# Optimization experiments

Hardware: AMD Instinct MI355X
Metric: run time of the kernel (lower is better)

Reference implementation:

```python
import jax, jax.numpy as jnp
import numpy as np

H = 64          # hidden_dim
G = 4           # grid_size
NB = 4.0        # neighborhood
PRED = 12       # pred_steps


def _social_pool(all_h, positions, idx, W_sp, b_sp):
    """Vectorized grid-based social pooling. all_h:(N,H), positions:(N,2) -> (H,)."""
    N = positions.shape[0]
    pos_i = positions[idx]
    diff = positions - pos_i                                   # (N,2)
    in_nb = jnp.max(jnp.abs(diff), axis=1) <= NB
    mask = in_nb & (jnp.arange(N) != idx)
    # torch: int(clamp(((d/NB)+1)/2 * G, 0, G-1)); truncation==floor after clip here
    g = jnp.clip(jnp.floor((diff / NB + 1.0) / 2.0 * G), 0, G - 1).astype(jnp.int32)
    cell = g[:, 1] * G + g[:, 0]                               # gy*G + gx, (N,)
    m = mask.astype(all_h.dtype)[:, None]                      # (N,1)
    grid = jax.ops.segment_sum(all_h * m, cell, num_segments=G * G)   # (16,H)
    counts = jax.ops.segment_sum(m, cell, num_segments=G * G)         # (16,1)
    pooled = (grid / jnp.maximum(counts, 1.0)).sum(axis=0)            # (H,)
    return pooled @ W_sp.T + b_sp


def _lstm_cell(inp, h, c, W_ih, b_ih, W_hh, b_hh):
    gates = inp @ W_ih.T + b_ih + h @ W_hh.T + b_hh            # (4H,)
    i, f, g, o = jnp.split(gates, 4)
    i, f, o = jax.nn.sigmoid(i), jax.nn.sigmoid(f), jax.nn.sigmoid(o)
    g = jnp.tanh(g)
    c_new = f * c + i * g
    return o * jnp.tanh(c_new), c_new


def setup_inputs() -> dict:
    key = jax.random.key(0)
    ks = jax.random.split(key, 10)
    N, T = 2_000_000, 8
    s = 0.05
    return {
        "history": jax.random.normal(ks[0], (T, 4), jnp.float32),
        "all_h": jax.random.normal(ks[1], (N, H), jnp.float32),
        "positions": jax.random.normal(ks[2], (N, 2), jnp.float32) * 3.0,
        "W_in": jax.random.normal(ks[3], (H, 4), jnp.float32) * s,
        "b_in": jnp.zeros((H,), jnp.float32),
        "W_ih": jax.random.normal(ks[4], (4 * H, 2 * H), jnp.float32) * s,
        "b_ih": jnp.zeros((4 * H,), jnp.float32),
        "W_hh": jax.random.normal(ks[5], (4 * H, H), jnp.float32) * s,
        "b_hh": jnp.zeros((4 * H,), jnp.float32),
        "W_sp": jax.random.normal(ks[6], (H, H), jnp.float32) * s,
        "b_sp": jnp.zeros((H,), jnp.float32),
        "W_out": jax.random.normal(ks[7], (2, H), jnp.float32) * s,
        "b_out": jnp.zeros((2,), jnp.float32),
        "idx": 0,
    }


def reference(history, all_h, positions, W_in, b_in, W_ih, b_ih, W_hh, b_hh,
              W_sp, b_sp, W_out, b_out, idx):
    # all_h, positions, idx are fixed inputs, so the social vector is identical
    # at every timestep (same math as recomputing it each step in the original).
    social = _social_pool(all_h, positions, idx, W_sp, b_sp)   # (H,)

    def enc_step(carry, x):
        h, c = carry
        emb = x @ W_in.T + b_in
        inp = jnp.concatenate([emb, social])
        h, c = _lstm_cell(inp, h, c, W_ih, b_ih, W_hh, b_hh)
        return (h, c), None

    h0 = jnp.zeros((H,), history.dtype)
    (h, c), _ = jax.lax.scan(enc_step, (h0, h0), history)

    last_pos = history[-1, :2]

    def pred_step(carry, _):
        h, c, lp = carry
        delta = h @ W_out.T + b_out                            # (2,)
        vel = delta / 0.5
        x = jnp.concatenate([lp + delta, vel])                 # (4,)
        emb = x @ W_in.T + b_in
        inp = jnp.concatenate([emb, social])
        h, c = _lstm_cell(inp, h, c, W_ih, b_ih, W_hh, b_hh)
        return (h, c, lp + delta), delta

    _, preds = jax.lax.scan(pred_step, (h, c, last_pos), None, length=PRED)
    return preds  # (pred_steps, 2)
```

## Files before the change

kernel.cpp:

```cpp
#include <hip/hip_runtime.h>

#define HDIM 64
#define CELLS 16
#define WPB 4
#define PV (CELLS * HDIM + CELLS)

#define WS_M1K   1040
#define WS_G0    2064
#define WS_SINK  2320
#define WS_PART  2576

__global__ void __launch_bounds__(256) k_pool(
    const float* __restrict__ all_h, const float2* __restrict__ pos2,
    const int* __restrict__ idxp, float* __restrict__ partial,
    int N, int nwaves)
{
    __shared__ float acc[WPB][CELLS * HDIM];
    __shared__ float cnt[WPB][CELLS];
    __shared__ __align__(16) int lst[WPB][64];
    const int tid  = threadIdx.x;
    const int wave = tid >> 6;
    const int lane = tid & 63;

    for (int v = tid; v < WPB * CELLS * HDIM; v += 256) ((float*)acc)[v] = 0.0f;
    if (tid < WPB * CELLS) ((float*)cnt)[tid] = 0.0f;
    __syncthreads();

    const int    idx0 = idxp[0];
    const float2 p0   = pos2[idx0];
    const int    gw   = blockIdx.x * WPB + wave;
    float* __restrict__ accw = acc[wave];
    int*   __restrict__ lstw = lst[wave];

    for (int base = gw * 64; base < N; base += nwaves * 64) {
        const int a = base + lane;
        int cellid = -1;
        if (a < N && a != idx0) {
            const float2 p = pos2[a];
            const float dx = p.x - p0.x;
            const float dy = p.y - p0.y;
            if (fmaxf(fabsf(dx), fabsf(dy)) <= 4.0f) {
                const float f0 = floorf((dx / 4.0f + 1.0f) / 2.0f * 4.0f);
                const float f1 = floorf((dy / 4.0f + 1.0f) / 2.0f * 4.0f);
                const int g0 = (int)fminf(fmaxf(f0, 0.0f), 3.0f);
                const int g1 = (int)fminf(fmaxf(f1, 0.0f), 3.0f);
                cellid = g1 * 4 + g0;
                atomicAdd(&cnt[wave][cellid], 1.0f);
            }
        }
        const unsigned long long mask  = __ballot(cellid >= 0);
        const int                M     = __popcll(mask);
        const unsigned long long below = mask & ((1ULL << lane) - 1ULL);
        if (cellid >= 0) lstw[__popcll(below)] = (lane << 4) | cellid;

        const float* __restrict__ rowp = all_h + (size_t)base * HDIM + lane;
        int r = 0;
        for (; r + 16 <= M; r += 16) {
            const int4 e0 = *(const int4*)&lstw[r];
            const int4 e1 = *(const int4*)&lstw[r + 4];
            const int4 e2 = *(const int4*)&lstw[r + 8];
            const int4 e3 = *(const int4*)&lstw[r + 12];
            const float v0  = rowp[(size_t)(e0.x >> 4) * HDIM];
            const float v1  = rowp[(size_t)(e0.y >> 4) * HDIM];
            const float v2  = rowp[(size_t)(e0.z >> 4) * HDIM];
            const float v3  = rowp[(size_t)(e0.w >> 4) * HDIM];
            const float v4  = rowp[(size_t)(e1.x >> 4) * HDIM];
            const float v5  = rowp[(size_t)(e1.y >> 4) * HDIM];
            const float v6  = rowp[(size_t)(e1.z >> 4) * HDIM];
            const float v7  = rowp[(size_t)(e1.w >> 4) * HDIM];
            const float v8  = rowp[(size_t)(e2.x >> 4) * HDIM];
            const float v9  = rowp[(size_t)(e2.y >> 4) * HDIM];
            const float v10 = rowp[(size_t)(e2.z >> 4) * HDIM];
            const float v11 = rowp[(size_t)(e2.w >> 4) * HDIM];
            const float v12 = rowp[(size_t)(e3.x >> 4) * HDIM];
            const float v13 = rowp[(size_t)(e3.y >> 4) * HDIM];
            const float v14 = rowp[(size_t)(e3.z >> 4) * HDIM];
            const float v15 = rowp[(size_t)(e3.w >> 4) * HDIM];
            accw[(e0.x & 15) * HDIM + lane] += v0;
            accw[(e0.y & 15) * HDIM + lane] += v1;
            accw[(e0.z & 15) * HDIM + lane] += v2;
            accw[(e0.w & 15) * HDIM + lane] += v3;
            accw[(e1.x & 15) * HDIM + lane] += v4;
            accw[(e1.y & 15) * HDIM + lane] += v5;
            accw[(e1.z & 15) * HDIM + lane] += v6;
            accw[(e1.w & 15) * HDIM + lane] += v7;
            accw[(e2.x & 15) * HDIM + lane] += v8;
            accw[(e2.y & 15) * HDIM + lane] += v9;
            accw[(e2.z & 15) * HDIM + lane] += v10;
            accw[(e2.w & 15) * HDIM + lane] += v11;
            accw[(e3.x & 15) * HDIM + lane] += v12;
            accw[(e3.y & 15) * HDIM + lane] += v13;
            accw[(e3.z & 15) * HDIM + lane] += v14;
            accw[(e3.w & 15) * HDIM + lane] += v15;
        }
        for (; r + 8 <= M; r += 8) {
            const int4 e0 = *(const int4*)&lstw[r];
            const int4 e1 = *(const int4*)&lstw[r + 4];
            const float v0 = rowp[(size_t)(e0.x >> 4) * HDIM];
            const float v1 = rowp[(size_t)(e0.y >> 4) * HDIM];
            const float v2 = rowp[(size_t)(e0.z >> 4) * HDIM];
            const float v3 = rowp[(size_t)(e0.w >> 4) * HDIM];
            const float v4 = rowp[(size_t)(e1.x >> 4) * HDIM];
            const float v5 = rowp[(size_t)(e1.y >> 4) * HDIM];
            const float v6 = rowp[(size_t)(e1.z >> 4) * HDIM];
            const float v7 = rowp[(size_t)(e1.w >> 4) * HDIM];
            accw[(e0.x & 15) * HDIM + lane] += v0;
            accw[(e0.y & 15) * HDIM + lane] += v1;
            accw[(e0.z & 15) * HDIM + lane] += v2;
            accw[(e0.w & 15) * HDIM + lane] += v3;
            accw[(e1.x & 15) * HDIM + lane] += v4;
            accw[(e1.y & 15) * HDIM + lane] += v5;
            accw[(e1.z & 15) * HDIM + lane] += v6;
            accw[(e1.w & 15) * HDIM + lane] += v7;
        }
        for (; r < M; ++r) {
            const int e = lstw[r];
            accw[(e & 15) * HDIM + lane] += rowp[(size_t)(e >> 4) * HDIM];
        }
    }
    __syncthreads();

    float* __restrict__ outp = partial + (size_t)blockIdx.x * PV;
    for (int v = tid; v < CELLS * HDIM; v += 256)
        outp[v] = acc[0][v] + acc[1][v] + acc[2][v] + acc[3][v];
    if (tid < CELLS)
        outp[CELLS * HDIM + tid] = cnt[0][tid] + cnt[1][tid] + cnt[2][tid] + cnt[3][tid];
}

__global__ void __launch_bounds__(256) k_reduce(
    const float* __restrict__ partial, float* __restrict__ ws,
    const float* __restrict__ W_in, const float* __restrict__ b_in,
    const float* __restrict__ W_ih, const float* __restrict__ b_ih,
    const float* __restrict__ W_hh, const float* __restrict__ b_hh,
    const float* __restrict__ W_sp, const float* __restrict__ W_out,
    int nbp)
{
    const int tid = threadIdx.x;
    if (blockIdx.x < 260) {
        const int wave = tid >> 6;
        const int lane = tid & 63;
        const int v = blockIdx.x * 4 + wave;
        if (v >= PV) return;
        float s = 0.0f;
        for (int b = lane; b < nbp; b += 64)
            s += partial[(size_t)b * PV + v];
        #pragma unroll
        for (int off = 32; off > 0; off >>= 1)
            s += __shfl_xor(s, off);
        if (lane == 0) ws[v] = s;
        return;
    }
    float m0 = 0.0f, m1 = 0.0f, m2 = 0.0f, m3 = 0.0f;
    float gc = b_ih[tid] + b_hh[tid];
    for (int m = 0; m < 64; m += 4) {
        const float4 w4 = *(const float4*)&W_ih[tid * 128 + m];
        const float4 a0 = *(const float4*)&W_in[m * 4];
        const float4 a1 = *(const float4*)&W_in[(m + 1) * 4];
        const float4 a2 = *(const float4*)&W_in[(m + 2) * 4];
        const float4 a3 = *(const float4*)&W_in[(m + 3) * 4];
        m0 += w4.x * a0.x + w4.y * a1.x + w4.z * a2.x + w4.w * a3.x;
        m1 += w4.x * a0.y + w4.y * a1.y + w4.z * a2.y + w4.w * a3.y;
        m2 += w4.x * a0.z + w4.y * a1.z + w4.z * a2.z + w4.w * a3.z;
        m3 += w4.x * a0.w + w4.y * a1.w + w4.z * a2.w + w4.w * a3.w;
        gc += w4.x * b_in[m] + w4.y * b_in[m + 1]
            + w4.z * b_in[m + 2] + w4.w * b_in[m + 3];
    }
    float4 mv; mv.x = m0; mv.y = m1; mv.z = m2; mv.w = m3;
    *(float4*)&ws[WS_M1K + tid * 4] = mv;
    ws[WS_G0 + tid] = gc;
    float warm = 0.0f;
    for (int k = 0; k < 64; k += 4) {
        const float4 a = *(const float4*)&W_ih[tid * 128 + 64 + k];
        const float4 b = *(const float4*)&W_hh[tid * 64 + k];
        warm += a.x + a.y + a.z + a.w + b.x + b.y + b.z + b.w;
    }
    for (int k = 0; k < 16; k += 4) {
        const float4 c = *(const float4*)&W_sp[tid * 16 + k];
        warm += c.x + c.y + c.z + c.w;
    }
    warm += W_out[tid & 127];
    ws[WS_SINK + tid] = warm;
}

__global__ void __launch_bounds__(256) k_lstm(
    const float* __restrict__ ws, const float* __restrict__ history,
    const float* __restrict__ W_ih, const float* __restrict__ W_hh,
    const float* __restrict__ W_sp, const float* __restrict__ b_sp,
    const float* __restrict__ W_out, const float* __restrict__ b_out,
    float* __restrict__ out)
{
    __shared__ __align__(16) float pooled[64];
    __shared__ __align__(16) float social[64];
    __shared__ __align__(16) float hl[64];
    __shared__ __align__(16) float cl[64];
    __shared__ float gl[256];
    __shared__ __align__(16) float histl[32];
    __shared__ float xs[4];
    __shared__ float lp[2];
    const int tid = threadIdx.x;

    if (tid < 32) histl[tid] = history[tid];
    if (tid < 64) {
        float p = 0.0f;
        #pragma unroll
        for (int c = 0; c < CELLS; ++c) {
            const float cc = ws[CELLS * HDIM + c];
            p += ws[c * HDIM + tid] / fmaxf(cc, 1.0f);
        }
        pooled[tid] = p;
    }
    __syncthreads();
    if (tid < 64) {
        float s = b_sp[tid];
        for (int k = 0; k < 64; k += 4) {
            const float4 w4 = *(const float4*)&W_sp[tid * 64 + k];
            s += pooled[k] * w4.x + pooled[k + 1] * w4.y
               + pooled[k + 2] * w4.z + pooled[k + 3] * w4.w;
        }
        social[tid] = s;
        hl[tid] = 0.0f;
        cl[tid] = 0.0f;
    }
    if (tid == 0) { lp[0] = histl[28]; lp[1] = histl[29]; }
    __syncthreads();

    const float4 mv = *(const float4*)&ws[WS_M1K + tid * 4];
    float gconst = ws[WS_G0 + tid];
    for (int k = 0; k < 64; k += 4) {
        const float4 w4 = *(const float4*)&W_ih[tid * 128 + 64 + k];
        gconst += w4.x * social[k] + w4.y * social[k + 1]
                + w4.z * social[k + 2] + w4.w * social[k + 3];
    }
    float whh[64];
    #pragma unroll
    for (int k = 0; k < 64; k += 4) {
        const float4 w4 = *(const float4*)&W_hh[tid * 64 + k];
        whh[k] = w4.x; whh[k + 1] = w4.y; whh[k + 2] = w4.z; whh[k + 3] = w4.w;
    }
    float wout0 = 0.0f, wout1 = 0.0f, bo0 = 0.0f, bo1 = 0.0f;
    if (tid < 64) {
        wout0 = W_out[tid]; wout1 = W_out[64 + tid];
        bo0 = b_out[0]; bo1 = b_out[1];
    }
    __syncthreads();

    for (int t = 0; t < 8; ++t) {
        const float x0 = histl[t * 4 + 0], x1 = histl[t * 4 + 1];
        const float x2 = histl[t * 4 + 2], x3 = histl[t * 4 + 3];
        float g0 = gconst + mv.x * x0 + mv.y * x1;
        float g1 = mv.z * x2 + mv.w * x3;
        float g2 = 0.0f, g3 = 0.0f;
        #pragma unroll
        for (int k = 0; k < 64; k += 16) {
            const float4 a = *(const float4*)&hl[k];
            const float4 b = *(const float4*)&hl[k + 4];
            const float4 c = *(const float4*)&hl[k + 8];
            const float4 d = *(const float4*)&hl[k + 12];
            g0 += whh[k] * a.x + whh[k + 1] * a.y + whh[k + 2] * a.z + whh[k + 3] * a.w;
            g1 += whh[k + 4] * b.x + whh[k + 5] * b.y + whh[k + 6] * b.z + whh[k + 7] * b.w;
            g2 += whh[k + 8] * c.x + whh[k + 9] * c.y + whh[k + 10] * c.z + whh[k + 11] * c.w;
            g3 += whh[k + 12] * d.x + whh[k + 13] * d.y + whh[k + 14] * d.z + whh[k + 15] * d.w;
        }
        gl[tid] = (g0 + g1) + (g2 + g3);
        __syncthreads();
        if (tid < 64) {
            const float ig = 1.0f / (1.0f + expf(-gl[tid]));
            const float fg = 1.0f / (1.0f + expf(-gl[64 + tid]));
            const float gg = tanhf(gl[128 + tid]);
            const float og = 1.0f / (1.0f + expf(-gl[192 + tid]));
            const float cn = fg * cl[tid] + ig * gg;
            cl[tid] = cn;
            hl[tid] = og * tanhf(cn);
        }
        __syncthreads();
    }

    for (int t = 0; t < 12; ++t) {
        if (tid < 64) {
            float s0 = wout0 * hl[tid];
            float s1 = wout1 * hl[tid];
            #pragma unroll
            for (int off = 32; off > 0; off >>= 1) {
                s0 += __shfl_xor(s0, off);
                s1 += __shfl_xor(s1, off);
            }
            if (tid == 0) {
                const float d0 = s0 + bo0, d1 = s1 + bo1;
                out[t * 2 + 0] = d0;
                out[t * 2 + 1] = d1;
                const float n0 = lp[0] + d0, n1 = lp[1] + d1;
                xs[0] = n0; xs[1] = n1;
                xs[2] = d0 * 2.0f; xs[3] = d1 * 2.0f;
                lp[0] = n0; lp[1] = n1;
            }
        }
        __syncthreads();
        const float x0 = xs[0], x1 = xs[1], x2 = xs[2], x3 = xs[3];
        float g0 = gconst + mv.x * x0 + mv.y * x1;
        float g1 = mv.z * x2 + mv.w * x3;
        float g2 = 0.0f, g3 = 0.0f;
        #pragma unroll
        for (int k = 0; k < 64; k += 16) {
            const float4 a = *(const float4*)&hl[k];
            const float4 b = *(const float4*)&hl[k + 4];
            const float4 c = *(const float4*)&hl[k + 8];
            const float4 d = *(const float4*)&hl[k + 12];
            g0 += whh[k] * a.x + whh[k + 1] * a.y + whh[k + 2] * a.z + whh[k + 3] * a.w;
            g1 += whh[k + 4] * b.x + whh[k + 5] * b.y + whh[k + 6] * b.z + whh[k + 7] * b.w;
            g2 += whh[k + 8] * c.x + whh[k + 9] * c.y + whh[k + 10] * c.z + whh[k + 11] * c.w;
            g3 += whh[k + 12] * d.x + whh[k + 13] * d.y + whh[k + 14] * d.z + whh[k + 15] * d.w;
        }
        gl[tid] = (g0 + g1) + (g2 + g3);
        __syncthreads();
        if (tid < 64) {
            const float ig = 1.0f / (1.0f + expf(-gl[tid]));
            const float fg = 1.0f / (1.0f + expf(-gl[64 + tid]));
            const float gg = tanhf(gl[128 + tid]);
            const float og = 1.0f / (1.0f + expf(-gl[192 + tid]));
            const float cn = fg * cl[tid] + ig * gg;
            cl[tid] = cn;
            hl[tid] = og * tanhf(cn);
        }
        __syncthreads();
    }
}

extern "C" void kernel_launch(void* const* d_in, const int* in_sizes, int n_in,
                              void* d_out, int out_size, void* d_ws, size_t ws_size,
                              hipStream_t stream) {
    const float* history   = (const float*)d_in[0];
    const float* all_h     = (const float*)d_in[1];
    const float* positions = (const float*)d_in[2];
    const float* W_in  = (const float*)d_in[3];
    const float* b_in  = (const float*)d_in[4];
    const float* W_ih  = (const float*)d_in[5];
    const float* b_ih  = (const float*)d_in[6];
    const float* W_hh  = (const float*)d_in[7];
    const float* b_hh  = (const float*)d_in[8];
    const float* W_sp  = (const float*)d_in[9];
    const float* b_sp  = (const float*)d_in[10];
    const float* W_out = (const float*)d_in[11];
    const float* b_out = (const float*)d_in[12];
    const int*   idxp  = (const int*)d_in[13];
    const int N = in_sizes[2] / 2;

    float* ws      = (float*)d_ws;
    float* partial = ws + WS_PART;

    long long avail = (long long)(ws_size / sizeof(float)) - WS_PART;
    int nbp = 2048;
    if ((long long)nbp * PV > avail) nbp = (int)(avail / PV);
    if (nbp < 1) nbp = 1;

    k_pool<<<nbp, 256, 0, stream>>>(all_h, (const float2*)positions, idxp,
                                    partial, N, nbp * WPB);
    k_reduce<<<261, 256, 0, stream>>>(partial, ws, W_in, b_in, W_ih, b_ih,
                                      W_hh, b_hh, W_sp, W_out, nbp);
    k_lstm<<<1, 256, 0, stream>>>(ws, history, W_ih, W_hh, W_sp, b_sp,
                                  W_out, b_out, (float*)d_out);
}
```

Measured before the change: 74.06 us.

## Restructure pool gather into contiguous ranges with float4 row loads and compaction

The pooling kernel now gives each wave a contiguous slice of agents, prefetches the next positions, and builds a compacted list of in-neighbourhood agents that persists across iterations. The list is drained 16 rows at a time, with each quarter-wave loading a whole 64-float row as float4 and adding it into padded shared accumulators with LDS atomics. The reduce kernel reads the partials as float4, so it launches far fewer blocks. This targets uncoalesced scalar gathers and poorly filled batches when few agents are neighbours. In exchange it adds shared-memory atomic contention and a list capacity bound of 96 entries per wave.

```diff
diff --git a/kernel.cpp b/kernel.cpp
--- a/kernel.cpp
+++ b/kernel.cpp
@@ -1,42 +1,57 @@
 #include <hip/hip_runtime.h>
 
-#define HDIM 64
+#define HDIM  64
 #define CELLS 16
-#define WPB 4
-#define PV (CELLS * HDIM + CELLS)
-
-#define WS_M1K   1040
-#define WS_G0    2064
-#define WS_SINK  2320
-#define WS_PART  2576
-
-__global__ void __launch_bounds__(256) k_pool(
+#define ASTR  65
+#define WPB   4
+#define PV    (CELLS * HDIM + CELLS)
+#define LCAP  96
+
+#define WS_M1K  1040
+#define WS_G0   2064
+#define WS_SINK 2320
+#define WS_PART 2576
+
+__global__ void __launch_bounds__(256, 4) k_pool(
     const float* __restrict__ all_h, const float2* __restrict__ pos2,
     const int* __restrict__ idxp, float* __restrict__ partial,
     int N, int nwaves)
 {
-    __shared__ float acc[WPB][CELLS * HDIM];
+    __shared__ float acc[WPB][CELLS * ASTR];
     __shared__ float cnt[WPB][CELLS];
-    __shared__ __align__(16) int lst[WPB][64];
+    __shared__ int   lst[WPB][LCAP];
     const int tid  = threadIdx.x;
     const int wave = tid >> 6;
     const int lane = tid & 63;
 
-    for (int v = tid; v < WPB * CELLS * HDIM; v += 256) ((float*)acc)[v] = 0.0f;
+    for (int v = tid; v < WPB * CELLS * ASTR; v += 256) ((float*)acc)[v] = 0.0f;
     if (tid < WPB * CELLS) ((float*)cnt)[tid] = 0.0f;
     __syncthreads();
 
     const int    idx0 = idxp[0];
     const float2 p0   = pos2[idx0];
     const int    gw   = blockIdx.x * WPB + wave;
+    const int a0 = (int)((long long)gw * N / nwaves);
+    const int a1 = (int)((long long)(gw + 1) * N / nwaves);
     float* __restrict__ accw = acc[wave];
+    float* __restrict__ cntw = cnt[wave];
     int*   __restrict__ lstw = lst[wave];
 
-    for (int base = gw * 64; base < N; base += nwaves * 64) {
+    const int grp  = lane >> 4;
+    const int colb = lane & 15;
+    int cnt_n = 0;
+
+    float2 pn = (a0 + lane < a1) ? pos2[a0 + lane] : make_float2(1e30f, 1e30f);
+
+    for (int base = a0; base < a1; base += 64) {
+        const float2 p = pn;
+        const int nb = base + 64;
+        if (nb < a1)
+            pn = (nb + lane < a1) ? pos2[nb + lane] : make_float2(1e30f, 1e30f);
+
         const int a = base + lane;
         int cellid = -1;
-        if (a < N && a != idx0) {
-            const float2 p = pos2[a];
+        if (a < a1 && a != idx0) {
             const float dx = p.x - p0.x;
             const float dy = p.y - p0.y;
             if (fmaxf(fabsf(dx), fabsf(dy)) <= 4.0f) {
@@ -45,84 +60,78 @@
                 const int g0 = (int)fminf(fmaxf(f0, 0.0f), 3.0f);
                 const int g1 = (int)fminf(fmaxf(f1, 0.0f), 3.0f);
                 cellid = g1 * 4 + g0;
-                atomicAdd(&cnt[wave][cellid], 1.0f);
-            }
-        }
-        const unsigned long long mask  = __ballot(cellid >= 0);
-        const int                M     = __popcll(mask);
-        const unsigned long long below = mask & ((1ULL << lane) - 1ULL);
-        if (cellid >= 0) lstw[__popcll(below)] = (lane << 4) | cellid;
-
-        const float* __restrict__ rowp = all_h + (size_t)base * HDIM + lane;
-        int r = 0;
-        for (; r + 16 <= M; r += 16) {
-            const int4 e0 = *(const int4*)&lstw[r];
-            const int4 e1 = *(const int4*)&lstw[r + 4];
-            const int4 e2 = *(const int4*)&lstw[r + 8];
-            const int4 e3 = *(const int4*)&lstw[r + 12];
-            const float v0  = rowp[(size_t)(e0.x >> 4) * HDIM];
-            const float v1  = rowp[(size_t)(e0.y >> 4) * HDIM];
-            const float v2  = rowp[(size_t)(e0.z >> 4) * HDIM];
-            const float v3  = rowp[(size_t)(e0.w >> 4) * HDIM];
-            const float v4  = rowp[(size_t)(e1.x >> 4) * HDIM];
-            const float v5  = rowp[(size_t)(e1.y >> 4) * HDIM];
-            const float v6  = rowp[(size_t)(e1.z >> 4) * HDIM];
-            const float v7  = rowp[(size_t)(e1.w >> 4) * HDIM];
-            const float v8  = rowp[(size_t)(e2.x >> 4) * HDIM];
-            const float v9  = rowp[(size_t)(e2.y >> 4) * HDIM];
-            const float v10 = rowp[(size_t)(e2.z >> 4) * HDIM];
-            const float v11 = rowp[(size_t)(e2.w >> 4) * HDIM];
-            const float v12 = rowp[(size_t)(e3.x >> 4) * HDIM];
-            const float v13 = rowp[(size_t)(e3.y >> 4) * HDIM];
-            const float v14 = rowp[(size_t)(e3.z >> 4) * HDIM];
-            const float v15 = rowp[(size_t)(e3.w >> 4) * HDIM];
-            accw[(e0.x & 15) * HDIM + lane] += v0;
-            accw[(e0.y & 15) * HDIM + lane] += v1;
-            accw[(e0.z & 15) * HDIM + lane] += v2;
-            accw[(e0.w & 15) * HDIM + lane] += v3;
-            accw[(e1.x & 15) * HDIM + lane] += v4;
-            accw[(e1.y & 15) * HDIM + lane] += v5;
-            accw[(e1.z & 15) * HDIM + lane] += v6;
-            accw[(e1.w & 15) * HDIM + lane] += v7;
-            accw[(e2.x & 15) * HDIM + lane] += v8;
-            accw[(e2.y & 15) * HDIM + lane] += v9;
-            accw[(e2.z & 15) * HDIM + lane] += v10;
-            accw[(e2.w & 15) * HDIM + lane] += v11;
-            accw[(e3.x & 15) * HDIM + lane] += v12;
-            accw[(e3.y & 15) * HDIM + lane] += v13;
-            accw[(e3.z & 15) * HDIM + lane] += v14;
-            accw[(e3.w & 15) * HDIM + lane] += v15;
-        }
-        for (; r + 8 <= M; r += 8) {
-            const int4 e0 = *(const int4*)&lstw[r];
-            const int4 e1 = *(const int4*)&lstw[r + 4];
-            const float v0 = rowp[(size_t)(e0.x >> 4) * HDIM];
-            const float v1 = rowp[(size_t)(e0.y >> 4) * HDIM];
-            const float v2 = rowp[(size_t)(e0.z >> 4) * HDIM];
-            const float v3 = rowp[(size_t)(e0.w >> 4) * HDIM];
-            const float v4 = rowp[(size_t)(e1.x >> 4) * HDIM];
-            const float v5 = rowp[(size_t)(e1.y >> 4) * HDIM];
-            const float v6 = rowp[(size_t)(e1.z >> 4) * HDIM];
-            const float v7 = rowp[(size_t)(e1.w >> 4) * HDIM];
-            accw[(e0.x & 15) * HDIM + lane] += v0;
-            accw[(e0.y & 15) * HDIM + lane] += v1;
-            accw[(e0.z & 15) * HDIM + lane] += v2;
-            accw[(e0.w & 15) * HDIM + lane] += v3;
-            accw[(e1.x & 15) * HDIM + lane] += v4;
-            accw[(e1.y & 15) * HDIM + lane] += v5;
-            accw[(e1.z & 15) * HDIM + lane] += v6;
-            accw[(e1.w & 15) * HDIM + lane] += v7;
-        }
-        for (; r < M; ++r) {
-            const int e = lstw[r];
-            accw[(e & 15) * HDIM + lane] += rowp[(size_t)(e >> 4) * HDIM];
+                atomicAdd(&cntw[cellid], 1.0f);
+            }
+        }
+        const unsigned long long m = __ballot(cellid >= 0);
+        if (cellid >= 0) {
+            const int pos = cnt_n + __popcll(m & ((1ULL << lane) - 1ULL));
+            lstw[pos] = (a << 4) | cellid;
+        }
+        cnt_n += __popcll(m);
+
+        while (cnt_n >= 16) {
+            cnt_n -= 16;
+            float4 v0, v1, v2, v3;
+            int c0, c1, c2, c3;
+            {
+                const int e = lstw[cnt_n + 0 * 4 + grp];
+                c0 = e & 15;
+                v0 = ((const float4*)(all_h + ((size_t)(e >> 4) << 6)))[colb];
+            }
+            {
+                const int e = lstw[cnt_n + 1 * 4 + grp];
+                c1 = e & 15;
+                v1 = ((const float4*)(all_h + ((size_t)(e >> 4) << 6)))[colb];
+            }
+            {
+                const int e = lstw[cnt_n + 2 * 4 + grp];
+                c2 = e & 15;
+                v2 = ((const float4*)(all_h + ((size_t)(e >> 4) << 6)))[colb];
+            }
+            {
+                const int e = lstw[cnt_n + 3 * 4 + grp];
+                c3 = e & 15;
+                v3 = ((const float4*)(all_h + ((size_t)(e >> 4) << 6)))[colb];
+            }
+            float* a0p = accw + c0 * ASTR + colb * 4;
+            atomicAdd(a0p + 0, v0.x); atomicAdd(a0p + 1, v0.y);
+            atomicAdd(a0p + 2, v0.z); atomicAdd(a0p + 3, v0.w);
+            float* a1p = accw + c1 * ASTR + colb * 4;
+            atomicAdd(a1p + 0, v1.x); atomicAdd(a1p + 1, v1.y);
+            atomicAdd(a1p + 2, v1.z); atomicAdd(a1p + 3, v1.w);
+            float* a2p = accw + c2 * ASTR + colb * 4;
+            atomicAdd(a2p + 0, v2.x); atomicAdd(a2p + 1, v2.y);
+            atomicAdd(a2p + 2, v2.z); atomicAdd(a2p + 3, v2.w);
+            float* a3p = accw + c3 * ASTR + colb * 4;
+            atomicAdd(a3p + 0, v3.x); atomicAdd(a3p + 1, v3.y);
+            atomicAdd(a3p + 2, v3.z); atomicAdd(a3p + 3, v3.w);
+        }
+    }
+
+    {
+        const int rem = cnt_n;
+        #pragma unroll
+        for (int j = 0; j < 4; ++j) {
+            const int r = j * 4 + grp;
+            if (r < rem) {
+                const int e = lstw[r];
+                const float4 vv =
+                    ((const float4*)(all_h + ((size_t)(e >> 4) << 6)))[colb];
+                float* ap = accw + (e & 15) * ASTR + colb * 4;
+                atomicAdd(ap + 0, vv.x); atomicAdd(ap + 1, vv.y);
+                atomicAdd(ap + 2, vv.z); atomicAdd(ap + 3, vv.w);
+            }
         }
     }
     __syncthreads();
 
     float* __restrict__ outp = partial + (size_t)blockIdx.x * PV;
-    for (int v = tid; v < CELLS * HDIM; v += 256)
-        outp[v] = acc[0][v] + acc[1][v] + acc[2][v] + acc[3][v];
+    for (int v = tid; v < CELLS * HDIM; v += 256) {
+        const int c = v >> 6, col = v & 63;
+        outp[v] = acc[0][c * ASTR + col] + acc[1][c * ASTR + col]
+                + acc[2][c * ASTR + col] + acc[3][c * ASTR + col];
+    }
     if (tid < CELLS)
         outp[CELLS * HDIM + tid] = cnt[0][tid] + cnt[1][tid] + cnt[2][tid] + cnt[3][tid];
 }
@@ -136,32 +145,41 @@
     int nbp)
 {
     const int tid = threadIdx.x;
-    if (blockIdx.x < 260) {
+    if (blockIdx.x < 65) {
         const int wave = tid >> 6;
         const int lane = tid & 63;
-        const int v = blockIdx.x * 4 + wave;
-        if (v >= PV) return;
-        float s = 0.0f;
-        for (int b = lane; b < nbp; b += 64)
-            s += partial[(size_t)b * PV + v];
-        #pragma unroll
-        for (int off = 32; off > 0; off >>= 1)
-            s += __shfl_xor(s, off);
-        if (lane == 0) ws[v] = s;
+        const int q = blockIdx.x * 4 + wave;
+        if (q * 4 >= PV) return;
+        float s0 = 0.0f, s1 = 0.0f, s2 = 0.0f, s3 = 0.0f;
+        for (int b = lane; b < nbp; b += 64) {
+            const float4 t = *(const float4*)&partial[(size_t)b * PV + q * 4];
+            s0 += t.x; s1 += t.y; s2 += t.z; s3 += t.w;
+        }
+        #pragma unroll
+        for (int off = 32; off > 0; off >>= 1) {
+            s0 += __shfl_xor(s0, off);
+            s1 += __shfl_xor(s1, off);
+            s2 += __shfl_xor(s2, off);
+            s3 += __shfl_xor(s3, off);
+        }
+        if (lane == 0) {
+            float4 r; r.x = s0; r.y = s1; r.z = s2; r.w = s3;
+            *(float4*)&ws[q * 4] = r;
+        }
         return;
     }
     float m0 = 0.0f, m1 = 0.0f, m2 = 0.0f, m3 = 0.0f;
     float gc = b_ih[tid] + b_hh[tid];
     for (int m = 0; m < 64; m += 4) {
         const float4 w4 = *(const float4*)&W_ih[tid * 128 + m];
-        const float4 a0 = *(const float4*)&W_in[m * 4];
-        const float4 a1 = *(const float4*)&W_in[(m + 1) * 4];
-        const float4 a2 = *(const float4*)&W_in[(m + 2) * 4];
-        const float4 a3 = *(const float4*)&W_in[(m + 3) * 4];
-        m0 += w4.x * a0.x + w4.y * a1.x + w4.z * a2.x + w4.w * a3.x;
-        m1 += w4.x * a0.y + w4.y * a1.y + w4.z * a2.y + w4.w * a3.y;
-        m2 += w4.x * a0.z + w4.y * a1.z + w4.z * a2.z + w4.w * a3.z;
-        m3 += w4.x * a0.w + w4.y * a1.w + w4.z * a2.w + w4.w * a3.w;
+        const float4 q0 = *(const float4*)&W_in[m * 4];
+        const float4 q1 = *(const float4*)&W_in[(m + 1) * 4];
+        const float4 q2 = *(const float4*)&W_in[(m + 2) * 4];
+        const float4 q3 = *(const float4*)&W_in[(m + 3) * 4];
+        m0 += w4.x * q0.x + w4.y * q1.x + w4.z * q2.x + w4.w * q3.x;
+        m1 += w4.x * q0.y + w4.y * q1.y + w4.z * q2.y + w4.w * q3.y;
+        m2 += w4.x * q0.z + w4.y * q1.z + w4.z * q2.z + w4.w * q3.z;
+        m3 += w4.x * q0.w + w4.y * q1.w + w4.z * q2.w + w4.w * q3.w;
         gc += w4.x * b_in[m] + w4.y * b_in[m + 1]
             + w4.z * b_in[m + 2] + w4.w * b_in[m + 3];
     }
@@ -354,8 +372,8 @@
 
     k_pool<<<nbp, 256, 0, stream>>>(all_h, (const float2*)positions, idxp,
                                     partial, N, nbp * WPB);
-    k_reduce<<<261, 256, 0, stream>>>(partial, ws, W_in, b_in, W_ih, b_ih,
-                                      W_hh, b_hh, W_sp, W_out, nbp);
+    k_reduce<<<66, 256, 0, stream>>>(partial, ws, W_in, b_in, W_ih, b_ih,
+                                     W_hh, b_hh, W_sp, W_out, nbp);
     k_lstm<<<1, 256, 0, stream>>>(ws, history, W_ih, W_hh, W_sp, b_sp,
                                   W_out, b_out, (float*)d_out);
 }
```

New measurement: 215.5 us. 191% more time.
